# Performance work log

Hardware: AMD Instinct MI355X
Metric: run time of the kernel (lower is better)

The kernel has to match this reference:

```python
import jax, jax.numpy as jnp
import numpy as np

B, N, F_DIM = 32, 1024, 128
ALPHA = 0.2        # LeakyReLU negative slope
PAD = -9e15        # pad_sequence padding value in the original
DENSITY = 0.05


def setup_inputs() -> dict:
    key = jax.random.key(0)
    k1, k2, k3 = jax.random.split(key, 3)
    # sparse 0/1 adjacency with self-loops so every node has degree >= 1
    adj = (jax.random.uniform(k1, (B, N, N)) < DENSITY).astype(jnp.float32)
    eye = jnp.eye(N, dtype=jnp.float32)[None, :, :]
    adj = jnp.maximum(adj, eye)
    feats = jax.random.normal(k2, (B, N, F_DIM), dtype=jnp.float32)
    # xavier_uniform with leaky_relu gain on a [2F, 1]
    gain = float(np.sqrt(2.0 / (1.0 + ALPHA ** 2)))
    bound = gain * float(np.sqrt(6.0 / (2 * F_DIM + 1)))
    a = jax.random.uniform(k3, (2 * F_DIM, 1), minval=-bound, maxval=bound,
                           dtype=jnp.float32)
    return {"batch_graphs": adj, "batch_features": feats, "a": a}


def reference(batch_graphs, batch_features, a):
    # e_ij = LeakyReLU([h_i || h_j] @ a) decomposes as (h_i @ a1) + (h_j @ a2)
    s_src = batch_features @ a[:F_DIM, 0]   # [B, N] contribution of node i
    s_dst = batch_features @ a[F_DIM:, 0]   # [B, N] contribution of neighbor j
    e = s_src[:, :, None] + s_dst[:, None, :]            # [B, N, N]
    e = jnp.where(e >= 0, e, ALPHA * e)                   # LeakyReLU
    mask = batch_graphs == 1
    e = jnp.where(mask, e, PAD)                           # pad non-edges like pad_sequence
    att = jax.nn.softmax(e, axis=-1)                      # segmented softmax over neighbors
    att = jnp.where(mask, att, 0.0)                       # scatter back only real edges
    return att
```

## Files before the change

kernel.cpp:

```cpp
#include <hip/hip_runtime.h>
#include <hip/hip_bf16.h>
#include <stdint.h>

#define B_DIM 32
#define N_DIM 1024
#define F_DIM 128
#define ALPHA 0.2f
#define NROWS (B_DIM * N_DIM)
#define TAIL_ROWS 128
#define MAIN_ROWS (NROWS - TAIL_ROWS)
#define SCORE_BYTES ((size_t)(2 * NROWS) * sizeof(float))

typedef float          vf4 __attribute__((ext_vector_type(4)));
typedef unsigned short vh4 __attribute__((ext_vector_type(4)));
typedef unsigned int   vu4 __attribute__((ext_vector_type(4)));

__device__ __forceinline__ unsigned short f32_to_bf16_bits(float f) {
    union { __hip_bfloat16 h; unsigned short u; } cvt;
    cvt.h = __float2bfloat16(f);
    return cvt.u;
}

__device__ __forceinline__ bool probe_is_f32(const void* adj) {
    return *(const uint32_t*)adj == 0x3F800000u;
}

template <bool F32>
__device__ __forceinline__ float* score_base(void* out) {
    const size_t out_bytes = (size_t)NROWS * N_DIM * (F32 ? 4 : 2);
    return (float*)((char*)out + out_bytes - SCORE_BYTES);
}

template <bool F32>
__device__ __forceinline__ void scores_body(
    const void* __restrict__ feats_v, const void* __restrict__ a_v, void* out)
{
    float* base  = score_base<F32>(out);
    float* s_src = base;
    float* s_dst = base + NROWS;

    const int wid  = threadIdx.x >> 6;
    const int lane = threadIdx.x & 63;
    const int row  = blockIdx.x * 4 + wid;
    const int f0   = lane * 2;

    float x0, x1, a10, a11, a20, a21;
    if (F32) {
        const float* fp = (const float*)feats_v + (size_t)row * F_DIM + f0;
        const float* ap = (const float*)a_v;
        x0 = fp[0]; x1 = fp[1];
        a10 = ap[f0];         a11 = ap[f0 + 1];
        a20 = ap[F_DIM + f0]; a21 = ap[F_DIM + f0 + 1];
    } else {
        const __hip_bfloat16* fp = (const __hip_bfloat16*)feats_v + (size_t)row * F_DIM + f0;
        const __hip_bfloat16* ap = (const __hip_bfloat16*)a_v;
        x0  = __bfloat162float(fp[0]);           x1  = __bfloat162float(fp[1]);
        a10 = __bfloat162float(ap[f0]);          a11 = __bfloat162float(ap[f0 + 1]);
        a20 = __bfloat162float(ap[F_DIM + f0]);  a21 = __bfloat162float(ap[F_DIM + f0 + 1]);
    }

    float v1 = x0 * a10 + x1 * a11;
    float v2 = x0 * a20 + x1 * a21;
    #pragma unroll
    for (int off = 32; off > 0; off >>= 1) {
        v1 += __shfl_down(v1, off, 64);
        v2 += __shfl_down(v2, off, 64);
    }
    if (lane == 0) { s_src[row] = v1; s_dst[row] = v2; }
}

__global__ __launch_bounds__(256) void scores_kernel(
    const void* __restrict__ adj, const void* __restrict__ feats,
    const void* __restrict__ a, void* out)
{
    if (probe_is_f32(adj)) scores_body<true>(feats, a, out);
    else                   scores_body<false>(feats, a, out);
}

template <bool F32>
__device__ __forceinline__ void wave_softmax_row(
    const void* __restrict__ adj_v, void* __restrict__ out_v,
    int row, float ssrc, const float* __restrict__ sdst )
{
    const int lane = threadIdx.x & 63;

    float p[16];
    uint32_t vmask = 0;
    float lmax = -1e30f;

    #pragma unroll
    for (int c = 0; c < 4; ++c) {
        const int idx = c * 64 + lane;
        const vf4 sd = ((const vf4*)sdst)[idx];
        bool v[4];
        if (F32) {
            const vu4 av = ((const vu4*)((const float*)adj_v + (size_t)row * N_DIM))[idx];
            v[0] = av.x != 0u; v[1] = av.y != 0u; v[2] = av.z != 0u; v[3] = av.w != 0u;
        } else {
            const vh4 av = ((const vh4*)((const __hip_bfloat16*)adj_v + (size_t)row * N_DIM))[idx];
            v[0] = av.x != 0; v[1] = av.y != 0; v[2] = av.z != 0; v[3] = av.w != 0;
        }
        const float sdk[4] = {sd.x, sd.y, sd.z, sd.w};
        #pragma unroll
        for (int k = 0; k < 4; ++k) {
            float t = ssrc + sdk[k];
            t = (t >= 0.0f) ? t : ALPHA * t;
            p[c * 4 + k] = t;
            if (v[k]) { lmax = fmaxf(lmax, t); vmask |= 1u << (c * 4 + k); }
        }
    }

    #pragma unroll
    for (int off = 1; off < 64; off <<= 1)
        lmax = fmaxf(lmax, __shfl_xor(lmax, off, 64));

    float lsum = 0.0f;
    #pragma unroll
    for (int i = 0; i < 16; ++i) {
        p[i] = (vmask >> i) & 1 ? __expf(p[i] - lmax) : 0.0f;
        lsum += p[i];
    }
    #pragma unroll
    for (int off = 1; off < 64; off <<= 1)
        lsum += __shfl_xor(lsum, off, 64);
    const float inv = 1.0f / lsum;

    #pragma unroll
    for (int c = 0; c < 4; ++c) {
        const int idx = c * 64 + lane;
        if (F32) {
            vf4 o;
            o.x = p[c*4+0] * inv; o.y = p[c*4+1] * inv;
            o.z = p[c*4+2] * inv; o.w = p[c*4+3] * inv;
            ((vf4*)((float*)out_v + (size_t)row * N_DIM))[idx] = o;
        } else {
            vh4 o;
            o.x = f32_to_bf16_bits(p[c*4+0] * inv);
            o.y = f32_to_bf16_bits(p[c*4+1] * inv);
            o.z = f32_to_bf16_bits(p[c*4+2] * inv);
            o.w = f32_to_bf16_bits(p[c*4+3] * inv);
            ((vh4*)((__hip_bfloat16*)out_v + (size_t)row * N_DIM))[idx] = o;
        }
    }
}

template <bool F32>
__device__ __forceinline__ void main_body(const void* __restrict__ adj_v, void* out_v)
{
    const int wid = threadIdx.x >> 6;
    const int row = blockIdx.x * 4 + wid;
    const int b   = row >> 10;

    const float* base = score_base<F32>(out_v);
    const float  ssrc = base[row];
    const float* sdst = base + NROWS + (size_t)b * N_DIM;

    wave_softmax_row<F32>(adj_v, out_v, row, ssrc, sdst);
}

__global__ __launch_bounds__(256) void main_kernel(
    const void* __restrict__ adj, void* out)
{
    if (probe_is_f32(adj)) main_body<true>(adj, out);
    else                   main_body<false>(adj, out);
}

template <bool F32>
__device__ __forceinline__ void tail_body(
    const void* __restrict__ adj_v, const void* __restrict__ feats_v,
    const void* __restrict__ a_v, void* __restrict__ out_v)
{
    __shared__ float sdst_sh[N_DIM];

    const int tid  = threadIdx.x;
    const int wid  = tid >> 6;
    const int lane = tid & 63;
    const int b    = B_DIM - 1;
    const int row  = MAIN_ROWS + blockIdx.x * 4 + wid;

    #pragma unroll
    for (int k = 0; k < 4; ++k) {
        const int j = tid * 4 + k;
        float acc = 0.0f;
        if (F32) {
            const vf4* fp = (const vf4*)((const float*)feats_v + ((size_t)b * N_DIM + j) * F_DIM);
            const vf4* ap = (const vf4*)((const float*)a_v + F_DIM);
            #pragma unroll 8
            for (int f = 0; f < F_DIM / 4; ++f) {
                const vf4 x = fp[f], w = ap[f];
                acc += x.x * w.x + x.y * w.y + x.z * w.z + x.w * w.w;
            }
        } else {
            const __hip_bfloat16* fp = (const __hip_bfloat16*)feats_v + ((size_t)b * N_DIM + j) * F_DIM;
            const __hip_bfloat16* ap = (const __hip_bfloat16*)a_v + F_DIM;
            #pragma unroll 8
            for (int f = 0; f < F_DIM; ++f)
                acc += __bfloat162float(fp[f]) * __bfloat162float(ap[f]);
        }
        sdst_sh[j] = acc;
    }

    float ssrc;
    {
        const int f0 = lane * 2;
        float x0, x1, a0, a1;
        if (F32) {
            const float* fp = (const float*)feats_v + (size_t)row * F_DIM + f0;
            const float* ap = (const float*)a_v;
            x0 = fp[0]; x1 = fp[1]; a0 = ap[f0]; a1 = ap[f0 + 1];
        } else {
            const __hip_bfloat16* fp = (const __hip_bfloat16*)feats_v + (size_t)row * F_DIM + f0;
            const __hip_bfloat16* ap = (const __hip_bfloat16*)a_v;
            x0 = __bfloat162float(fp[0]); x1 = __bfloat162float(fp[1]);
            a0 = __bfloat162float(ap[f0]); a1 = __bfloat162float(ap[f0 + 1]);
        }
        float v = x0 * a0 + x1 * a1;
        #pragma unroll
        for (int off = 32; off > 0; off >>= 1)
            v += __shfl_down(v, off, 64);
        ssrc = __shfl(v, 0, 64);
    }
    __syncthreads();

    wave_softmax_row<F32>(adj_v, out_v, row, ssrc, sdst_sh);
}

__global__ __launch_bounds__(256) void tail_kernel(
    const void* __restrict__ adj, const void* __restrict__ feats,
    const void* __restrict__ a, void* __restrict__ out)
{
    if (probe_is_f32(adj)) tail_body<true>(adj, feats, a, out);
    else                   tail_body<false>(adj, feats, a, out);
}

extern "C" void kernel_launch(void* const* d_in, const int* in_sizes, int n_in,
                              void* d_out, int out_size, void* d_ws, size_t ws_size,
                              hipStream_t stream) {
    const void* adj   = d_in[0];
    const void* feats = d_in[1];
    const void* a     = d_in[2];
    (void)d_ws; (void)ws_size;

    scores_kernel<<<NROWS / 4, 256, 0, stream>>>(adj, feats, a, d_out);
    main_kernel<<<MAIN_ROWS / 4, 256, 0, stream>>>(adj, d_out);
    tail_kernel<<<TAIL_ROWS / 4, 256, 0, stream>>>(adj, feats, a, d_out);
}
```

Before: 262.2 us.

## Drop max subtraction and split softmax into separate sum and map kernels

Removes the row-max pass from the softmax, computing exp of the raw LeakyReLU scores directly. A separate sum kernel writes per-row inverse sums into scratch space at the end of the output, and a map kernel with one block per row rewrites the normalized values. The tail region grows to cover the extra scratch. This gives up overflow safety and re-reads the adjacency matrix, adding an extra full pass of memory traffic over a bandwidth-bound workload in exchange for simpler per-thread work and higher parallelism.

```diff
diff --git a/kernel.cpp b/kernel.cpp
--- a/kernel.cpp
+++ b/kernel.cpp
@@ -7,9 +7,9 @@
 #define F_DIM 128
 #define ALPHA 0.2f
 #define NROWS (B_DIM * N_DIM)
-#define TAIL_ROWS 128
+#define TAIL_ROWS 192
 #define MAIN_ROWS (NROWS - TAIL_ROWS)
-#define SCORE_BYTES ((size_t)(2 * NROWS) * sizeof(float))
+#define SCORE_BYTES ((size_t)(3 * NROWS) * sizeof(float))
 
 typedef float          vf4 __attribute__((ext_vector_type(4)));
 typedef unsigned short vh4 __attribute__((ext_vector_type(4)));
@@ -30,6 +30,8 @@
     const size_t out_bytes = (size_t)NROWS * N_DIM * (F32 ? 4 : 2);
     return (float*)((char*)out + out_bytes - SCORE_BYTES);
 }
+
+__device__ __forceinline__ float leaky(float t) { return fmaxf(t, ALPHA * t); }
 
 template <bool F32>
 __device__ __forceinline__ void scores_body(
@@ -78,20 +80,23 @@
 }
 
 template <bool F32>
-__device__ __forceinline__ void wave_softmax_row(
-    const void* __restrict__ adj_v, void* __restrict__ out_v,
-    int row, float ssrc, const float* __restrict__ sdst )
-{
+__device__ __forceinline__ void sum_body(const void* __restrict__ adj_v, void* out_v)
+{
+    const int wid  = threadIdx.x >> 6;
     const int lane = threadIdx.x & 63;
-
-    float p[16];
-    uint32_t vmask = 0;
-    float lmax = -1e30f;
-
+    const int row  = blockIdx.x * 4 + wid;
+    const int b    = row >> 10;
+
+    float* base = score_base<F32>(out_v);
+    const float  ssrc = base[row];
+    const float* sdst = base + NROWS + (size_t)b * N_DIM;
+
+    float lsum = 0.0f;
     #pragma unroll
     for (int c = 0; c < 4; ++c) {
         const int idx = c * 64 + lane;
         const vf4 sd = ((const vf4*)sdst)[idx];
+        const float sdk[4] = {sd.x, sd.y, sd.z, sd.w};
         bool v[4];
         if (F32) {
             const vu4 av = ((const vu4*)((const float*)adj_v + (size_t)row * N_DIM))[idx];
@@ -100,69 +105,68 @@
             const vh4 av = ((const vh4*)((const __hip_bfloat16*)adj_v + (size_t)row * N_DIM))[idx];
             v[0] = av.x != 0; v[1] = av.y != 0; v[2] = av.z != 0; v[3] = av.w != 0;
         }
-        const float sdk[4] = {sd.x, sd.y, sd.z, sd.w};
         #pragma unroll
-        for (int k = 0; k < 4; ++k) {
-            float t = ssrc + sdk[k];
-            t = (t >= 0.0f) ? t : ALPHA * t;
-            p[c * 4 + k] = t;
-            if (v[k]) { lmax = fmaxf(lmax, t); vmask |= 1u << (c * 4 + k); }
-        }
-    }
-
-    #pragma unroll
-    for (int off = 1; off < 64; off <<= 1)
-        lmax = fmaxf(lmax, __shfl_xor(lmax, off, 64));
-
-    float lsum = 0.0f;
-    #pragma unroll
-    for (int i = 0; i < 16; ++i) {
-        p[i] = (vmask >> i) & 1 ? __expf(p[i] - lmax) : 0.0f;
-        lsum += p[i];
-    }
+        for (int k = 0; k < 4; ++k)
+            lsum += v[k] ? __expf(leaky(ssrc + sdk[k])) : 0.0f;
+    }
+
     #pragma unroll
     for (int off = 1; off < 64; off <<= 1)
         lsum += __shfl_xor(lsum, off, 64);
-    const float inv = 1.0f / lsum;
-
-    #pragma unroll
-    for (int c = 0; c < 4; ++c) {
-        const int idx = c * 64 + lane;
-        if (F32) {
-            vf4 o;
-            o.x = p[c*4+0] * inv; o.y = p[c*4+1] * inv;
-            o.z = p[c*4+2] * inv; o.w = p[c*4+3] * inv;
-            ((vf4*)((float*)out_v + (size_t)row * N_DIM))[idx] = o;
-        } else {
-            vh4 o;
-            o.x = f32_to_bf16_bits(p[c*4+0] * inv);
-            o.y = f32_to_bf16_bits(p[c*4+1] * inv);
-            o.z = f32_to_bf16_bits(p[c*4+2] * inv);
-            o.w = f32_to_bf16_bits(p[c*4+3] * inv);
-            ((vh4*)((__hip_bfloat16*)out_v + (size_t)row * N_DIM))[idx] = o;
-        }
-    }
-}
-
-template <bool F32>
-__device__ __forceinline__ void main_body(const void* __restrict__ adj_v, void* out_v)
-{
-    const int wid = threadIdx.x >> 6;
-    const int row = blockIdx.x * 4 + wid;
+
+    if (lane == 0) (base + 2 * NROWS)[row] = 1.0f / lsum;
+}
+
+__global__ __launch_bounds__(256) void sum_kernel(
+    const void* __restrict__ adj, void* out)
+{
+    if (probe_is_f32(adj)) sum_body<true>(adj, out);
+    else                   sum_body<false>(adj, out);
+}
+
+template <bool F32>
+__device__ __forceinline__ void map_body(const void* __restrict__ adj_v, void* out_v)
+{
+    const int row = blockIdx.x;
     const int b   = row >> 10;
+    const int tid = threadIdx.x;
 
     const float* base = score_base<F32>(out_v);
     const float  ssrc = base[row];
-    const float* sdst = base + NROWS + (size_t)b * N_DIM;
-
-    wave_softmax_row<F32>(adj_v, out_v, row, ssrc, sdst);
-}
-
-__global__ __launch_bounds__(256) void main_kernel(
+    const float  iv   = (base + 2 * NROWS)[row];
+    const vf4    sd   = ((const vf4*)(base + NROWS + (size_t)b * N_DIM))[tid];
+    const float  sdk[4] = {sd.x, sd.y, sd.z, sd.w};
+
+    bool v[4];
+    if (F32) {
+        const vu4 av = ((const vu4*)((const float*)adj_v + (size_t)row * N_DIM))[tid];
+        v[0] = av.x != 0u; v[1] = av.y != 0u; v[2] = av.z != 0u; v[3] = av.w != 0u;
+    } else {
+        const vh4 av = ((const vh4*)((const __hip_bfloat16*)adj_v + (size_t)row * N_DIM))[tid];
+        v[0] = av.x != 0; v[1] = av.y != 0; v[2] = av.z != 0; v[3] = av.w != 0;
+    }
+
+    float q[4];
+    #pragma unroll
+    for (int k = 0; k < 4; ++k)
+        q[k] = v[k] ? __expf(leaky(ssrc + sdk[k])) * iv : 0.0f;
+
+    if (F32) {
+        vf4 o; o.x = q[0]; o.y = q[1]; o.z = q[2]; o.w = q[3];
+        ((vf4*)((float*)out_v + (size_t)row * N_DIM))[tid] = o;
+    } else {
+        vh4 o;
+        o.x = f32_to_bf16_bits(q[0]); o.y = f32_to_bf16_bits(q[1]);
+        o.z = f32_to_bf16_bits(q[2]); o.w = f32_to_bf16_bits(q[3]);
+        ((vh4*)((__hip_bfloat16*)out_v + (size_t)row * N_DIM))[tid] = o;
+    }
+}
+
+__global__ __launch_bounds__(256) void map_kernel(
     const void* __restrict__ adj, void* out)
 {
-    if (probe_is_f32(adj)) main_body<true>(adj, out);
-    else                   main_body<false>(adj, out);
+    if (probe_is_f32(adj)) map_body<true>(adj, out);
+    else                   map_body<false>(adj, out);
 }
 
 template <bool F32>
@@ -214,15 +218,57 @@
             x0 = __bfloat162float(fp[0]); x1 = __bfloat162float(fp[1]);
             a0 = __bfloat162float(ap[f0]); a1 = __bfloat162float(ap[f0 + 1]);
         }
-        float v = x0 * a0 + x1 * a1;
+        float s = x0 * a0 + x1 * a1;
         #pragma unroll
         for (int off = 32; off > 0; off >>= 1)
-            v += __shfl_down(v, off, 64);
-        ssrc = __shfl(v, 0, 64);
+            s += __shfl_down(s, off, 64);
+        ssrc = __shfl(s, 0, 64);
     }
     __syncthreads();
 
-    wave_softmax_row<F32>(adj_v, out_v, row, ssrc, sdst_sh);
+    float p[16], lsum = 0.0f;
+    #pragma unroll
+    for (int c = 0; c < 4; ++c) {
+        const int idx = c * 64 + lane;
+        const vf4 sd = ((const vf4*)sdst_sh)[idx];
+        const float sdk[4] = {sd.x, sd.y, sd.z, sd.w};
+        bool v[4];
+        if (F32) {
+            const vu4 av = ((const vu4*)((const float*)adj_v + (size_t)row * N_DIM))[idx];
+            v[0] = av.x != 0u; v[1] = av.y != 0u; v[2] = av.z != 0u; v[3] = av.w != 0u;
+        } else {
+            const vh4 av = ((const vh4*)((const __hip_bfloat16*)adj_v + (size_t)row * N_DIM))[idx];
+            v[0] = av.x != 0; v[1] = av.y != 0; v[2] = av.z != 0; v[3] = av.w != 0;
+        }
+        #pragma unroll
+        for (int k = 0; k < 4; ++k) {
+            const float q = v[k] ? __expf(leaky(ssrc + sdk[k])) : 0.0f;
+            p[c*4+k] = q;
+            lsum += q;
+        }
+    }
+    #pragma unroll
+    for (int off = 1; off < 64; off <<= 1)
+        lsum += __shfl_xor(lsum, off, 64);
+    const float inv = 1.0f / lsum;
+
+    #pragma unroll
+    for (int c = 0; c < 4; ++c) {
+        const int idx = c * 64 + lane;
+        if (F32) {
+            vf4 o;
+            o.x = p[c*4+0] * inv; o.y = p[c*4+1] * inv;
+            o.z = p[c*4+2] * inv; o.w = p[c*4+3] * inv;
+            ((vf4*)((float*)out_v + (size_t)row * N_DIM))[idx] = o;
+        } else {
+            vh4 o;
+            o.x = f32_to_bf16_bits(p[c*4+0] * inv);
+            o.y = f32_to_bf16_bits(p[c*4+1] * inv);
+            o.z = f32_to_bf16_bits(p[c*4+2] * inv);
+            o.w = f32_to_bf16_bits(p[c*4+3] * inv);
+            ((vh4*)((__hip_bfloat16*)out_v + (size_t)row * N_DIM))[idx] = o;
+        }
+    }
 }
 
 __global__ __launch_bounds__(256) void tail_kernel(
@@ -241,7 +287,8 @@
     const void* a     = d_in[2];
     (void)d_ws; (void)ws_size;
 
-    scores_kernel<<<NROWS / 4, 256, 0, stream>>>(adj, feats, a, d_out);
-    main_kernel<<<MAIN_ROWS / 4, 256, 0, stream>>>(adj, d_out);
-    tail_kernel<<<TAIL_ROWS / 4, 256, 0, stream>>>(adj, feats, a, d_out);
-}
+    scores_kernel<<<NROWS / 4,     256, 0, stream>>>(adj, feats, a, d_out);
+    sum_kernel   <<<MAIN_ROWS / 4, 256, 0, stream>>>(adj, d_out);
+    map_kernel   <<<MAIN_ROWS,     256, 0, stream>>>(adj, d_out);
+    tail_kernel  <<<TAIL_ROWS / 4, 256, 0, stream>>>(adj, feats, a, d_out);
+}
```

Result: slower. 276.7 us (+5.6%).
